# Kernel tuning notes

Measured on AMD Instinct MI355X. Metric: run time of the kernel, lower is better.

Reference implementation:

```python
import jax, jax.numpy as jnp
import numpy as np

N_R = 256          # number of relations
N_HOP_MAX = 3      # max hops
N_E = 200_000      # number of entities
N_T = 1_000_000    # number of KB triples
B = 32             # batch size
D_Q = 768          # BERT question embedding dim
D_IN = D_Q + (N_HOP_MAX - 1) * N_R  # input width of dense_inf / dense_att


def setup_inputs() -> dict:
    key = jax.random.key(0)
    ks = jax.random.split(key, 7)
    x = (jax.random.uniform(ks[0], (B, N_E)) < 0.001).astype(jnp.float32)
    h_q = jax.random.normal(ks[1], (B, D_Q), jnp.float32)
    W_inf = jax.random.normal(ks[2], (N_R, D_IN), jnp.float32) * 0.02
    W_att = jax.random.normal(ks[3], (1, D_IN), jnp.float32) * 0.02
    subj_idx = jax.random.randint(ks[4], (N_T,), 0, N_E, jnp.int32)
    rel_idx = jax.random.randint(ks[5], (N_T,), 0, N_R, jnp.int32)
    obj_idx = jax.random.randint(ks[6], (N_T,), 0, N_E, jnp.int32)
    return {"x": x, "h_q": h_q, "W_inf": W_inf, "W_att": W_att,
            "subj_idx": subj_idx, "rel_idx": rel_idx, "obj_idx": obj_idx,
            "n_hop": N_HOP_MAX}


def _one_step(x, r, subj_idx, rel_idx, obj_idx):
    # Equivalent to ((x @ M_subj.T) * (r @ M_rel.T)) @ M_obj with 0/1
    # indicator matrices: gather - elementwise multiply - scatter-add.
    x_t = jnp.take(x, subj_idx, axis=1)   # (B, N_T)
    r_t = jnp.take(r, rel_idx, axis=1)    # (B, N_T)
    prod = x_t * r_t                       # (B, N_T)
    # scatter-add over triples into object entities: (N_T, B) -> (N_E, B)
    return jax.ops.segment_sum(prod.T, obj_idx, num_segments=x.shape[1]).T


def reference(x, h_q, W_inf, W_att, subj_idx, rel_idx, obj_idx, n_hop):
    rs, cs, xs = [], [], []
    for i in range(n_hop):
        if i:
            # most-recent relation first, then older ones (rs[::-1])
            concat = jnp.concatenate([h_q] + rs[::-1], axis=1)
        else:
            concat = h_q
        pad = jnp.zeros((h_q.shape[0], (N_HOP_MAX - 1 - i) * N_R), h_q.dtype)
        concat = jnp.concatenate([concat, pad], axis=1)  # (B, D_IN)
        r = concat @ W_inf.T   # (B, N_R)
        c = concat @ W_att.T   # (B, 1)
        x = _one_step(x, r, subj_idx, rel_idx, obj_idx)  # (B, N_E)
        rs.append(r)
        cs.append(c)
        xs.append(x)
    a = jax.nn.softmax(jnp.concatenate(cs, axis=1), axis=-1)  # (B, n_hop)
    y = jnp.einsum('bh,bhe->be', a, jnp.stack(xs, axis=1))     # (B, N_E)
    return y
```

## Files before the change

kernel.cpp:

```cpp
#include <hip/hip_runtime.h>

#define N_R   256
#define N_E   200000
#define N_T   1000000
#define D_Q   768
#define D_IN  1280

template <bool BN>
__device__ __forceinline__ void hop_core(
        const float* __restrict__ xIn, const unsigned* __restrict__ maskIn,
        const float* __restrict__ rT,
        const int* __restrict__ subj, const int* __restrict__ rel,
        const int* __restrict__ obj,
        float* __restrict__ xOut, unsigned* __restrict__ maskOut,
        int gb, int nGroups, int t) {
    int stride = nGroups * 256;
    for (int i = gb * 256 + t; i < N_T; i += stride) {
        int s = __builtin_nontemporal_load(&subj[i]);
        unsigned m = maskIn[s];
        if (!m) continue;
        int r = __builtin_nontemporal_load(&rel[i]);
        int o = __builtin_nontemporal_load(&obj[i]);
        const float* rrow = rT + r * 32;
        unsigned mm = m;
        while (mm) {
            int bb = __ffs(mm) - 1;
            mm &= mm - 1;
            float v = BN ? xIn[(size_t)bb * N_E + s] : xIn[(size_t)s * 32 + bb];
            unsafeAtomicAdd(&xOut[(size_t)o * 32 + bb], v * rrow[bb]);
        }
        atomicOr(&maskOut[o], m);
    }
}

__global__ void kA(const float* __restrict__ x, const float* __restrict__ h_q,
                   const float* __restrict__ W_inf,
                   unsigned* __restrict__ mask0, unsigned* __restrict__ mask1,
                   unsigned* __restrict__ mask2,
                   float4* __restrict__ outv, float* __restrict__ rT0) {
    __shared__ float hs[32 * 257];
    __shared__ float red[256];
    int t = threadIdx.x;
    if (blockIdx.x < 782) {
        int tid = blockIdx.x * 256 + t;
        float4 z = {0.f, 0.f, 0.f, 0.f};
        for (int i = tid; i < 1600000; i += 782 * 256) outv[i] = z;
        if (tid < N_E) {
            unsigned m = 0;
#pragma unroll 8
            for (int b = 0; b < 32; ++b)
                m |= (x[(size_t)b * N_E + tid] != 0.f ? 1u : 0u) << b;
            mask0[tid] = m;
            mask1[tid] = 0u;
            mask2[tid] = 0u;
        }
    } else {
        int rel = blockIdx.x - 782;
        int b = t & 31, kp = t >> 5;
        float acc = 0.f;
        for (int c = 0; c < 3; ++c) {
            __syncthreads();
#pragma unroll
            for (int i = 0; i < 32; ++i)
                hs[i * 257 + t] = h_q[i * D_Q + c * 256 + t];
            __syncthreads();
            const float* w = &W_inf[rel * D_IN + c * 256 + kp * 32];
#pragma unroll
            for (int i = 0; i < 32; ++i)
                acc += w[i] * hs[b * 257 + kp * 32 + i];
        }
        red[t] = acc;
        __syncthreads();
        if (t < 32) {
            float s = 0.f;
            for (int q = 0; q < 8; ++q) s += red[q * 32 + t];
            rT0[rel * 32 + t] = s;
        }
    }
}

__global__ void kB(const float* __restrict__ W_inf, const float* __restrict__ rT0,
                   float* __restrict__ rT1,
                   const float* __restrict__ x, const unsigned* __restrict__ mask0,
                   const int* __restrict__ subj, const int* __restrict__ rel,
                   const int* __restrict__ obj,
                   float* __restrict__ bufA, unsigned* __restrict__ mask1) {
    __shared__ float red[256];
    int t = threadIdx.x;
    if (blockIdx.x < 256) {
        int relb = blockIdx.x;
        int b = t & 31, jp = t >> 5;
        const float* w2 = &W_inf[relb * D_IN + D_Q];
        float acc = 0.f;
#pragma unroll 8
        for (int jj = 0; jj < 32; ++jj) {
            int j = jp * 32 + jj;
            acc += w2[j] * rT0[j * 32 + b];
        }
        red[t] = acc;
        __syncthreads();
        if (t < 32) {
            float s = rT0[relb * 32 + t];
            for (int q = 0; q < 8; ++q) s += red[q * 32 + t];
            rT1[relb * 32 + t] = s;
        }
    } else {
        hop_core<true>(x, mask0, rT0, subj, rel, obj, bufA, mask1,
                       blockIdx.x - 256, 2048, t);
    }
}

__global__ void kC(const float* __restrict__ W_inf, const float* __restrict__ W_att,
                   const float* __restrict__ h_q,
                   const float* __restrict__ rT0, const float* __restrict__ rT1,
                   float* __restrict__ rT2, float* __restrict__ a_w,
                   const float* __restrict__ bufA, const unsigned* __restrict__ mask1,
                   const int* __restrict__ subj, const int* __restrict__ rel,
                   const int* __restrict__ obj,
                   float* __restrict__ bufB, unsigned* __restrict__ mask2) {
    __shared__ float red[256];
    __shared__ float p0[256], p1[256], p2[256], p3[256];
    int t = threadIdx.x;
    if (blockIdx.x < 256) {
        int relb = blockIdx.x;
        int b = t & 31, jp = t >> 5;
        const float* w2 = &W_inf[relb * D_IN + D_Q];
        const float* w3 = w2 + N_R;
        float acc = 0.f;
#pragma unroll 8
        for (int jj = 0; jj < 32; ++jj) {
            int j = jp * 32 + jj;
            acc += w2[j] * rT1[j * 32 + b] + w3[j] * rT0[j * 32 + b];
        }
        red[t] = acc;
        __syncthreads();
        if (t < 32) {
            float s = rT0[relb * 32 + t];
            for (int q = 0; q < 8; ++q) s += red[q * 32 + t];
            rT2[relb * 32 + t] = s;
        }
    } else if (blockIdx.x == 256) {
        int b = t & 31, p = t >> 5;
        float c0 = 0.f;
        for (int k = p * 96; k < p * 96 + 96; ++k) c0 += W_att[k] * h_q[b * D_Q + k];
        float s1 = 0.f, s2 = 0.f, s3 = 0.f;
        for (int j = p * 32; j < p * 32 + 32; ++j) {
            float w2 = W_att[D_Q + j], w3 = W_att[D_Q + N_R + j];
            float r0v = rT0[j * 32 + b], r1v = rT1[j * 32 + b];
            s1 += w2 * r0v; s2 += w2 * r1v; s3 += w3 * r0v;
        }
        p0[t] = c0; p1[t] = s1; p2[t] = s2; p3[t] = s3;
        __syncthreads();
        if (t < 32) {
            float C0 = 0.f, S1 = 0.f, S2 = 0.f, S3 = 0.f;
            for (int q = 0; q < 8; ++q) {
                C0 += p0[q * 32 + t]; S1 += p1[q * 32 + t];
                S2 += p2[q * 32 + t]; S3 += p3[q * 32 + t];
            }
            float c1 = C0 + S1, c2 = C0 + S2 + S3;
            float m  = fmaxf(C0, fmaxf(c1, c2));
            float e0 = __expf(C0 - m), e1 = __expf(c1 - m), e2 = __expf(c2 - m);
            float inv = 1.f / (e0 + e1 + e2);
            a_w[t] = e0 * inv; a_w[32 + t] = e1 * inv; a_w[64 + t] = e2 * inv;
        }
    } else {
        hop_core<false>(bufA, mask1, rT1, subj, rel, obj, bufB, mask2,
                        blockIdx.x - 257, 2048, t);
    }
}

__global__ void kD(const float* __restrict__ bufB, const unsigned* __restrict__ mask2,
                   const float* __restrict__ rT2, const float* __restrict__ a_w,
                   const int* __restrict__ subj, const int* __restrict__ rel,
                   const int* __restrict__ obj, float* __restrict__ out) {
    __shared__ float aws[32];
    int t = threadIdx.x;
    if (t < 32) aws[t] = a_w[64 + t];
    __syncthreads();
    int stride = gridDim.x * 256;
    for (int i = blockIdx.x * 256 + t; i < N_T; i += stride) {
        int s = __builtin_nontemporal_load(&subj[i]);
        unsigned m = mask2[s];
        if (!m) continue;
        int r = __builtin_nontemporal_load(&rel[i]);
        int o = __builtin_nontemporal_load(&obj[i]);
        const float* rrow = rT2 + r * 32;
        unsigned mm = m;
        while (mm) {
            int bb = __ffs(mm) - 1;
            mm &= mm - 1;
            float v = bufB[(size_t)s * 32 + bb];
            unsafeAtomicAdd(&out[(size_t)bb * N_E + o], aws[bb] * v * rrow[bb]);
        }
    }
}

__global__ void kE(const float* __restrict__ bufA, const float* __restrict__ bufB,
                   const float* __restrict__ a_w, float* __restrict__ out) {
    __shared__ float tile[32 * 65];
    __shared__ float a0s[32], a1s[32];
    int t = threadIdx.x;
    if (t < 32) { a0s[t] = a_w[t]; a1s[t] = a_w[32 + t]; }
    __syncthreads();
    int e0 = blockIdx.x * 64;
#pragma unroll
    for (int i = 0; i < 8; ++i) {
        int o = i * 256 + t;
        int e = o >> 5, b = o & 31;
        size_t idx = (size_t)(e0 + e) * 32 + b;
        tile[b * 65 + e] = a0s[b] * bufA[idx] + a1s[b] * bufB[idx];
    }
    __syncthreads();
#pragma unroll
    for (int i = 0; i < 8; ++i) {
        int o = i * 256 + t;
        int b = o >> 6, e = o & 63;
        int oi = b * N_E + e0 + e;
        out[oi] += tile[b * 65 + e];
    }
}

extern "C" void kernel_launch(void* const* d_in, const int* in_sizes, int n_in,
                              void* d_out, int out_size, void* d_ws, size_t ws_size,
                              hipStream_t stream) {
    const float* x     = (const float*)d_in[0];
    const float* h_q   = (const float*)d_in[1];
    const float* W_inf = (const float*)d_in[2];
    const float* W_att = (const float*)d_in[3];
    const int*   subj  = (const int*)d_in[4];
    const int*   rel   = (const int*)d_in[5];
    const int*   obj   = (const int*)d_in[6];
    float* out = (float*)d_out;

    const size_t NEB = (size_t)N_E * 32;
    float*    bufA  = (float*)d_ws;
    float*    bufB  = bufA + NEB;
    float*    rT0   = bufB + NEB;
    float*    rT1   = rT0 + N_R * 32;
    float*    rT2   = rT1 + N_R * 32;
    float*    a_w   = rT2 + N_R * 32;
    unsigned* mask0 = (unsigned*)(a_w + 96);
    unsigned* mask1 = mask0 + N_E;
    unsigned* mask2 = mask1 + N_E;

    kA<<<782 + 256, 256, 0, stream>>>(x, h_q, W_inf, mask0, mask1, mask2,
                                      (float4*)out, rT0);
    kB<<<256 + 2048, 256, 0, stream>>>(W_inf, rT0, rT1, x, mask0,
                                       subj, rel, obj, bufA, mask1);
    kC<<<257 + 2048, 256, 0, stream>>>(W_inf, W_att, h_q, rT0, rT1, rT2, a_w,
                                       bufA, mask1, subj, rel, obj, bufB, mask2);
    kD<<<2048, 256, 0, stream>>>(bufB, mask2, rT2, a_w, subj, rel, obj, out);
    kE<<<3125, 256, 0, stream>>>(bufA, bufB, a_w, out);
}
```

Before: 204.3 us.

## Fuse final hop scatter and weighted combine into one kernel with int4 index loads

Merges the last-hop scatter kernel and the combine kernel into a single launch. The first 977 blocks each process four triples per thread through int4 loads of the subject, relation and object indices. The remaining blocks compute the weighted sum of the earlier hops and now add it into the output with atomics, because the two parts run at the same time. This saves one launch and its serialization gap and lets the combine traffic overlap the scatter, at the cost of extra atomics in the combine path.

Measured after the change: 203.2 us. About the same (-0.5%).

```diff
diff --git a/kernel.cpp b/kernel.cpp
--- a/kernel.cpp
+++ b/kernel.cpp
@@ -169,54 +169,62 @@
     }
 }
 
-__global__ void kD(const float* __restrict__ bufB, const unsigned* __restrict__ mask2,
-                   const float* __restrict__ rT2, const float* __restrict__ a_w,
-                   const int* __restrict__ subj, const int* __restrict__ rel,
-                   const int* __restrict__ obj, float* __restrict__ out) {
-    __shared__ float aws[32];
-    int t = threadIdx.x;
-    if (t < 32) aws[t] = a_w[64 + t];
-    __syncthreads();
-    int stride = gridDim.x * 256;
-    for (int i = blockIdx.x * 256 + t; i < N_T; i += stride) {
-        int s = __builtin_nontemporal_load(&subj[i]);
-        unsigned m = mask2[s];
-        if (!m) continue;
-        int r = __builtin_nontemporal_load(&rel[i]);
-        int o = __builtin_nontemporal_load(&obj[i]);
-        const float* rrow = rT2 + r * 32;
-        unsigned mm = m;
-        while (mm) {
-            int bb = __ffs(mm) - 1;
-            mm &= mm - 1;
-            float v = bufB[(size_t)s * 32 + bb];
-            unsafeAtomicAdd(&out[(size_t)bb * N_E + o], aws[bb] * v * rrow[bb]);
-        }
-    }
-}
-
-__global__ void kE(const float* __restrict__ bufA, const float* __restrict__ bufB,
-                   const float* __restrict__ a_w, float* __restrict__ out) {
+__global__ void kDE(const float* __restrict__ bufA, const float* __restrict__ bufB,
+                    const unsigned* __restrict__ mask2, const float* __restrict__ rT2,
+                    const float* __restrict__ a_w,
+                    const int4* __restrict__ subj4, const int4* __restrict__ rel4,
+                    const int4* __restrict__ obj4, float* __restrict__ out) {
     __shared__ float tile[32 * 65];
-    __shared__ float a0s[32], a1s[32];
-    int t = threadIdx.x;
-    if (t < 32) { a0s[t] = a_w[t]; a1s[t] = a_w[32 + t]; }
-    __syncthreads();
-    int e0 = blockIdx.x * 64;
-#pragma unroll
-    for (int i = 0; i < 8; ++i) {
-        int o = i * 256 + t;
-        int e = o >> 5, b = o & 31;
-        size_t idx = (size_t)(e0 + e) * 32 + b;
-        tile[b * 65 + e] = a0s[b] * bufA[idx] + a1s[b] * bufB[idx];
-    }
-    __syncthreads();
-#pragma unroll
-    for (int i = 0; i < 8; ++i) {
-        int o = i * 256 + t;
-        int b = o >> 6, e = o & 63;
-        int oi = b * N_E + e0 + e;
-        out[oi] += tile[b * 65 + e];
+    __shared__ float a0s[32], a1s[32], aws[32];
+    int t = threadIdx.x;
+    if (blockIdx.x < 977) {
+        if (t < 32) aws[t] = a_w[64 + t];
+        __syncthreads();
+        int tid = blockIdx.x * 256 + t;
+        if (tid >= N_T / 4) return;
+        int4 s4 = subj4[tid];
+        unsigned m0 = mask2[s4.x], m1 = mask2[s4.y];
+        unsigned m2 = mask2[s4.z], m3 = mask2[s4.w];
+        if (!(m0 | m1 | m2 | m3)) return;
+        int4 r4 = rel4[tid];
+        int4 o4 = obj4[tid];
+        int      ss[4] = {s4.x, s4.y, s4.z, s4.w};
+        unsigned mk[4] = {m0, m1, m2, m3};
+        int      rr[4] = {r4.x, r4.y, r4.z, r4.w};
+        int      oo[4] = {o4.x, o4.y, o4.z, o4.w};
+#pragma unroll
+        for (int k = 0; k < 4; ++k) {
+            unsigned mm = mk[k];
+            if (!mm) continue;
+            const float* rrow = rT2 + rr[k] * 32;
+            const float* xrow = bufB + (size_t)ss[k] * 32;
+            int o = oo[k];
+            while (mm) {
+                int bb = __ffs(mm) - 1;
+                mm &= mm - 1;
+                float v = xrow[bb];
+                unsafeAtomicAdd(&out[(size_t)bb * N_E + o],
+                                aws[bb] * v * rrow[bb]);
+            }
+        }
+    } else {
+        if (t < 32) { a0s[t] = a_w[t]; a1s[t] = a_w[32 + t]; }
+        __syncthreads();
+        int e0 = (blockIdx.x - 977) * 64;
+#pragma unroll
+        for (int i = 0; i < 8; ++i) {
+            int o = i * 256 + t;
+            int e = o >> 5, b = o & 31;
+            size_t idx = (size_t)(e0 + e) * 32 + b;
+            tile[b * 65 + e] = a0s[b] * bufA[idx] + a1s[b] * bufB[idx];
+        }
+        __syncthreads();
+#pragma unroll
+        for (int i = 0; i < 8; ++i) {
+            int o = i * 256 + t;
+            int b = o >> 6, e = o & 63;
+            unsafeAtomicAdd(&out[(size_t)b * N_E + e0 + e], tile[b * 65 + e]);
+        }
     }
 }
 
@@ -249,6 +257,7 @@
                                        subj, rel, obj, bufA, mask1);
     kC<<<257 + 2048, 256, 0, stream>>>(W_inf, W_att, h_q, rT0, rT1, rT2, a_w,
                                        bufA, mask1, subj, rel, obj, bufB, mask2);
-    kD<<<2048, 256, 0, stream>>>(bufB, mask2, rT2, a_w, subj, rel, obj, out);
-    kE<<<3125, 256, 0, stream>>>(bufA, bufB, a_w, out);
-}
+    kDE<<<977 + 3125, 256, 0, stream>>>(bufA, bufB, mask2, rT2, a_w,
+                                        (const int4*)subj, (const int4*)rel,
+                                        (const int4*)obj, out);
+}
```
